# Optimization experiments

Hardware: AMD Instinct MI355X
Metric: run time of the kernel (lower is better)

Reference implementation:

```python
import jax, jax.numpy as jnp
import numpy as np

B, N, DIM, H, DH, K = 4, 2048, 512, 6, 64, 16
KEEP_PROB = 0.9  # 1 - dropout_rate
LOG2PI = float(np.log(2.0 * np.pi))
LOG_PRIOR = float(np.log(1.0 / K))


def setup_inputs() -> dict:
    key = jax.random.key(0)
    ks = jax.random.split(key, 7)
    inputs_q = jax.random.normal(ks[0], (B, N, DIM), dtype=jnp.float32)
    # decoder-style causal mask, shape [B, 1, q_len, kv_len]
    causal = jnp.tril(jnp.ones((N, N), dtype=jnp.float32))
    mask = jnp.broadcast_to(causal[None, None], (B, 1, N, N))
    # dropout keep mask broadcast across the query dim: [B, H, 1, kv_len]
    keep = jax.random.bernoulli(ks[1], KEEP_PROB, (B, H, 1, N)).astype(jnp.float32)
    w_qkv = jax.random.normal(ks[2], (DIM, 3 * H * DH), dtype=jnp.float32) * 0.02
    w_out = jax.random.normal(ks[3], (H * DH, DIM), dtype=jnp.float32) * 0.02
    mu_lookup = jax.random.normal(ks[4], (K, DIM), dtype=jnp.float32)
    logvar_lookup = jax.random.normal(ks[5], (K, DIM), dtype=jnp.float32) * 0.1
    return {
        "inputs_q": inputs_q,
        "mask": mask,
        "keep": keep,
        "w_qkv": w_qkv,
        "w_out": w_out,
        "mu_lookup": mu_lookup,
        "logvar_lookup": logvar_lookup,
    }


def reference(inputs_q, mask, keep, w_qkv, w_out, mu_lookup, logvar_lookup):
    # --- MultiHeadDotProductAttention (self-attn path) ---
    qkv = (inputs_q @ w_qkv).reshape(B, N, 3, H, DH)  # [B,N,3,H,DH]
    q, k, v = qkv[:, :, 0], qkv[:, :, 1], qkv[:, :, 2]
    # bias: 0 where mask > 0, -1e10 elsewhere (note: no 1/sqrt(d) scaling, as in source)
    bias = jnp.where(mask > 0, 0.0, -1e10)
    attn_weights = jnp.einsum('bqhd,bkhd->bhqk', q, k) + bias  # [B,H,N,N]
    attn_weights = jax.nn.softmax(attn_weights, axis=-1)
    # broadcast dropout: mask shared across the query dim
    attn_weights = attn_weights * keep / KEEP_PROB
    attn_out = jnp.einsum('bhqk,bkhd->bqhd', attn_weights, v)
    attn_out = attn_out.reshape(B, N, H * DH) @ w_out  # [B,N,DIM]

    # --- GMM posterior approx q(y|x) ~= p(y|z) (approx_qy_x, vectorized over k) ---
    z = attn_out.mean(axis=1)  # pooled latent, [B,DIM]
    diff = z[:, None, :] - mu_lookup[None]  # [B,K,DIM]
    llh = -0.5 * jnp.sum(
        diff * diff / jnp.exp(logvar_lookup)[None] + logvar_lookup[None] + LOG2PI,
        axis=-1,
    )  # [B,K]
    logLogit_qy_x = llh + LOG_PRIOR
    qy_x = jax.nn.softmax(logLogit_qy_x, axis=1)  # [B,K]

    # combine mixture mean back in so both branches are live in one output
    return attn_out + (qy_x @ mu_lookup)[:, None, :]
```

## Files before the change

kernel.cpp:

```cpp
#include <hip/hip_runtime.h>
#include <cstdint>
#include <cstddef>

#define NH 6
#define NSEQ 2048
#define DIMD 512
#define BATCH 4
#define HD 384
#define LOG2PI_F 1.8378770664093453f
#define LOG2E_F 1.44269504f

typedef __attribute__((ext_vector_type(8))) short short8;
typedef __attribute__((ext_vector_type(8))) unsigned short ushort8;
typedef __attribute__((ext_vector_type(4))) unsigned short ushort4v;
typedef __attribute__((ext_vector_type(4))) float floatx4;
typedef __attribute__((ext_vector_type(2))) unsigned int uint2v;

__device__ inline unsigned short f2bf(float f){
  unsigned int u = __float_as_uint(f);
  u += 0x7FFFu + ((u>>16)&1u);
  return (unsigned short)(u>>16);
}

#define GLD16(gp, lp) __builtin_amdgcn_global_load_lds( \
  (const __attribute__((address_space(1))) void*)(gp), \
  (__attribute__((address_space(3))) void*)(lp), 16, 0, 0)

__global__ __launch_bounds__(256) void prep_kernel(
    const float* __restrict__ xq, const float* __restrict__ wq, const float* __restrict__ wo,
    unsigned short* __restrict__ xbf, unsigned short* __restrict__ wqT,
    unsigned short* __restrict__ woT, float* __restrict__ zA)
{
  __shared__ __attribute__((aligned(16))) unsigned short Ls[64*72];
  const int bid = blockIdx.x, t = threadIdx.x;
  if (bid < 4096){
    int i = bid*256 + t;
    floatx4 v = *(const floatx4*)(xq + (size_t)i*4);
    ushort4v r;
    #pragma unroll
    for(int j=0;j<4;j++) r[j] = f2bf(v[j]);
    *(ushort4v*)(xbf + (size_t)i*4) = r;
  } else if (bid < 4096+144+48){
    const bool isq = bid < 4096+144;
    const int j  = isq ? bid-4096 : bid-(4096+144);
    const int nx = isq ? 18 : 8;
    const int R  = isq ? 512 : 384, C = isq ? 1152 : 512;
    const float* src = isq ? wq : wo;
    unsigned short* dst = isq ? wqT : woT;
    const int x = j % nx, y = j / nx;
    const int n0 = x*64, d0 = y*64;
    const float scale = (isq && n0 < 384) ? LOG2E_F : 1.0f;
    const int r = t>>2, c0 = (t&3)*16;
    #pragma unroll
    for (int jj=0;jj<16;jj+=4){
      floatx4 v = *(const floatx4*)(src + (size_t)(d0+r)*C + n0 + c0 + jj);
      #pragma unroll
      for(int q=0;q<4;q++) Ls[r*72 + c0+jj+q] = f2bf(v[q]*scale);
    }
    __syncthreads();
    #pragma unroll
    for (int jj=0;jj<16;jj+=8){
      ushort8 o;
      #pragma unroll
      for(int q=0;q<8;q++) o[q] = Ls[(c0+jj+q)*72 + r];
      *(ushort8*)(dst + (size_t)(n0+r)*R + d0 + c0 + jj) = o;
    }
  } else {
    for (int i=t; i<BATCH*HD; i+=256) zA[i] = 0.f;
  }
}

__global__ __launch_bounds__(256) void gemm_qkv(
    const unsigned short* __restrict__ A,
    const unsigned short* __restrict__ Bt,
    const float* __restrict__ keep,
    unsigned short* __restrict__ Qo, unsigned short* __restrict__ Ko, unsigned short* __restrict__ Vt)
{
  __shared__ __attribute__((aligned(16))) unsigned short Cs[128*136];
  unsigned short* As = Cs;
  unsigned short* Bs = Cs + 128*64;
  const int tid = threadIdx.x;
  const int w = tid>>6, lane = tid&63;
  const int wr = w>>1, wc = w&1;
  const int quad = lane>>4, l16 = lane&15;
  const int by = blockIdx.y;
  const int tM = blockIdx.x*128, tN = by*128;
  const int r8 = lane>>3, c8 = (lane&7)*8;
  floatx4 acc[4][4];
  floatx4 zed = {0.f,0.f,0.f,0.f};
  #pragma unroll
  for (int i=0;i<4;i++)
    #pragma unroll
    for(int j=0;j<4;j++) acc[i][j] = zed;

  for (int k0=0; k0<512; k0+=64){
    #pragma unroll
    for (int i=0;i<4;i++){
      int row = w*32 + i*8;
      GLD16(A  + (size_t)(tM+row+r8)*512 + k0 + c8, As + row*64);
      GLD16(Bt + (size_t)(tN+row+r8)*512 + k0 + c8, Bs + row*64);
    }
    __syncthreads();
    #pragma unroll
    for (int kk=0; kk<64; kk+=32){
      short8 af[4], bf[4];
      #pragma unroll
      for(int mt=0;mt<4;mt++)
        af[mt] = *(const short8*)(As + (wr*64+mt*16+l16)*64 + kk + quad*8);
      #pragma unroll
      for(int nt=0;nt<4;nt++)
        bf[nt] = *(const short8*)(Bs + (wc*64+nt*16+l16)*64 + kk + quad*8);
      #pragma unroll
      for(int mt=0;mt<4;mt++)
        #pragma unroll
        for(int nt=0;nt<4;nt++)
          acc[mt][nt] = __builtin_amdgcn_mfma_f32_16x16x32_bf16(af[mt], bf[nt], acc[mt][nt], 0,0,0);
    }
    __syncthreads();
  }
  const int b = tM>>11;
  if (by < 6){
    #pragma unroll
    for(int mt=0;mt<4;mt++)
      #pragma unroll
      for(int nt=0;nt<4;nt++)
        #pragma unroll
        for(int r=0;r<4;r++)
          Cs[(wr*64+mt*16+quad*4+r)*132 + wc*64+nt*16+l16] = f2bf(acc[mt][nt][r]);
    __syncthreads();
    const int row = tid>>1, colh = (tid&1)*64;
    const int gcol0 = tN + colh;
    const int tq = gcol0/384, rem = gcol0 - tq*384, h = rem>>6;
    const int grow = tM + row, n = grow & 2047;
    unsigned short* dst = (tq==0 ? Qo : Ko) + ((size_t)((b*NH+h)*NSEQ+n))*64;
    #pragma unroll
    for(int j=0;j<8;j++)
      *(ushort8*)(dst + j*8) = *(const ushort8*)(Cs + row*132 + colh + j*8);
  } else {
    const int hbase = (by-6)*2;
    const float* kp = keep + (size_t)(b*NH + hbase + wc)*NSEQ + (tM & 2047);
    #pragma unroll
    for(int mt=0;mt<4;mt++){
      float kv[4];
      #pragma unroll
      for(int r=0;r<4;r++) kv[r] = kp[wr*64+mt*16+quad*4+r];
      #pragma unroll
      for(int nt=0;nt<4;nt++){
        int col = wc*64+nt*16+l16;
        int row = wr*64+mt*16+quad*4;
        unsigned int lo = (unsigned int)f2bf(acc[mt][nt][0]*kv[0]) | ((unsigned int)f2bf(acc[mt][nt][1]*kv[1])<<16);
        unsigned int hi = (unsigned int)f2bf(acc[mt][nt][2]*kv[2]) | ((unsigned int)f2bf(acc[mt][nt][3]*kv[3])<<16);
        uint2v v2 = {lo, hi};
        *(uint2v*)(Cs + (size_t)col*136 + row) = v2;
      }
    }
    __syncthreads();
    const int nu = tid & 15;
    #pragma unroll
    for(int vc0=0; vc0<128; vc0+=16){
      int vtcol = vc0 + (tid>>4);
      int h2 = hbase + (vtcol>>6), dh = vtcol & 63;
      unsigned short* dstv = Vt + ((size_t)((b*NH+h2)*64 + dh))*NSEQ + (tM & 2047) + nu*8;
      *(ushort8*)dstv = *(const ushort8*)(Cs + (size_t)vtcol*136 + nu*8);
    }
  }
}

__global__ __launch_bounds__(64,2) void attn_kernel(
    const unsigned short* __restrict__ Qg, const unsigned short* __restrict__ Kg,
    const unsigned short* __restrict__ VtG,
    unsigned short* __restrict__ atp,
    float* __restrict__ zA)
{
  __shared__ __attribute__((aligned(16))) unsigned short Ps[64*76];
  const int lane = threadIdx.x;
  const int quad = lane>>4, l16 = lane&15;
  const int bid = blockIdx.x;
  const int idx = bid>>3;
  const int bh  = (bid&7) + 8*(idx % 3);
  const int c   = 31 - idx/3;
  const int b = bh/NH, h = bh - b*NH;
  const unsigned short* Qb = Qg  + (size_t)bh*NSEQ*64;
  const unsigned short* Kb = Kg  + (size_t)bh*NSEQ*64;
  const unsigned short* Vb = VtG + (size_t)bh*64*NSEQ;
  const int q0 = c*64;
  const int nkt = c + 1;

  short8 qf[4][2];
  #pragma unroll
  for(int mt=0;mt<4;mt++)
    #pragma unroll
    for(int kc=0;kc<2;kc++)
      qf[mt][kc] = *(const short8*)(Qb + (size_t)(q0+mt*16+l16)*64 + kc*32 + quad*8);

  short8 onesf;
  #pragma unroll
  for(int j=0;j<8;j++) onesf[j] = (short)0x3F80;

  floatx4 O[4][4];
  floatx4 accl[4];
  floatx4 zed = {0.f,0.f,0.f,0.f};
  #pragma unroll
  for(int mt=0;mt<4;mt++){
    #pragma unroll
    for(int dt=0;dt<4;dt++) O[mt][dt] = zed;
    accl[mt] = zed;
  }

  short8 kf[4][2];
  #pragma unroll
  for(int nt=0;nt<4;nt++)
    #pragma unroll
    for(int kc=0;kc<2;kc++)
      kf[nt][kc] = *(const short8*)(Kb + (size_t)(nt*16+l16)*64 + kc*32 + quad*8);

  for (int kt=0; kt<nkt; kt++){
    const int kB = kt*64;
    short8 vf[2][4];
    const unsigned short* vp0 = Vb + kB;
    #pragma unroll
    for(int kh=0;kh<2;kh++)
      #pragma unroll
      for(int dt=0;dt<4;dt++)
        vf[kh][dt] = *(const short8*)(vp0 + (size_t)(dt*16+l16)*NSEQ + kh*32 + quad*8);

    const bool dia = (kt == nkt-1);
    floatx4 m12 = {-17.3123404907f,-17.3123404907f,-17.3123404907f,-17.3123404907f};
    floatx4 sacc[4];
    #pragma unroll
    for(int mt=0;mt<4;mt++){
      #pragma unroll
      for(int nt=0;nt<4;nt++) sacc[nt] = m12;
      #pragma unroll
      for(int nt=0;nt<4;nt++)
        #pragma unroll
        for(int kc=0;kc<2;kc++)
          sacc[nt] = __builtin_amdgcn_mfma_f32_16x16x32_bf16(qf[mt][kc], kf[nt][kc], sacc[nt], 0,0,0);
      #pragma unroll
      for(int nt=0;nt<4;nt++){
        int key = kB + nt*16 + l16;
        #pragma unroll
        for(int r=0;r<4;r++){
          float p = exp2f(sacc[nt][r]);
          if (dia) p = (key <= q0 + mt*16 + quad*4 + r) ? p : 0.f;
          Ps[(mt*16+quad*4+r)*76 + nt*16 + l16] = (unsigned short)(__float_as_uint(p)>>16);
        }
      }
    }
    if (kt+1 < nkt){
      const unsigned short* kp0 = Kb + (size_t)(kt+1)*64*64;
      #pragma unroll
      for(int nt=0;nt<4;nt++)
        #pragma unroll
        for(int kc=0;kc<2;kc++)
          kf[nt][kc] = *(const short8*)(kp0 + (size_t)(nt*16+l16)*64 + kc*32 + quad*8);
    }
    #pragma unroll
    for(int kh=0;kh<2;kh++){
      #pragma unroll
      for(int mt=0;mt<4;mt++){
        short8 pf = *(const short8*)(Ps + (mt*16+l16)*76 + kh*32 + quad*8);
        accl[mt] = __builtin_amdgcn_mfma_f32_16x16x32_bf16(pf, onesf, accl[mt], 0,0,0);
        #pragma unroll
        for(int dt=0;dt<4;dt++)
          O[mt][dt] = __builtin_amdgcn_mfma_f32_16x16x32_bf16(pf, vf[kh][dt], O[mt][dt], 0,0,0);
      }
    }
  }

  #pragma unroll
  for(int mt=0;mt<4;mt++){
    float sc2[4];
    #pragma unroll
    for(int r=0;r<4;r++) sc2[r] = (1.0f/0.9f) / accl[mt][r];
    #pragma unroll
    for(int dt=0;dt<4;dt++){
      float s = 0.f;
      #pragma unroll
      for(int r=0;r<4;r++){
        float v = O[mt][dt][r]*sc2[r];
        s += v;
        Ps[(mt*16+quad*4+r)*76 + dt*16 + l16] = f2bf(v);
      }
      atomicAdd(&zA[b*HD + h*64 + dt*16 + l16], s);
    }
  }
  unsigned short* dstp = atp + ((size_t)(b*NSEQ + q0 + lane))*HD + h*64;
  #pragma unroll
  for(int j=0;j<4;j++)
    *(ushort8*)(dstp + j*8) = *(const ushort8*)(Ps + lane*76 + j*8);
  #pragma unroll
  for(int j=4;j<8;j++)
    *(ushort8*)(dstp + j*8) = *(const ushort8*)(Ps + lane*76 + j*8);
}

__global__ __launch_bounds__(256) void gmm_kernel(
    const float* __restrict__ zA, const float* __restrict__ wo,
    const float* __restrict__ mu, const float* __restrict__ lv, float* __restrict__ c)
{
  __shared__ float zAs[HD];
  __shared__ float zs[DIMD];
  __shared__ float sh[16];
  __shared__ float qy[16];
  const int tid = threadIdx.x;
  const int b = blockIdx.x;
  for (int i=tid; i<HD; i+=256) zAs[i] = zA[b*HD + i];
  __syncthreads();
  for (int d=tid; d<DIMD; d+=256){
    float s = 0.f;
    for (int k=0; k<HD; k++) s += zAs[k]*wo[(size_t)k*DIMD + d];
    zs[d] = s * (1.0f/2048.0f);
  }
  __syncthreads();
  const int k = tid>>4, li = tid&15;
  float part = 0.f;
  for(int d=li; d<DIMD; d+=16){
    float m = mu[k*DIMD+d], l = lv[k*DIMD+d];
    float diff = zs[d] - m;
    part += diff*diff*__expf(-l) + l + LOG2PI_F;
  }
  #pragma unroll
  for(int off=8;off>=1;off>>=1) part += __shfl_xor(part, off, 64);
  if (li==0) sh[k] = part;
  __syncthreads();
  if (tid<16){
    float logit = -0.5f*sh[tid];
    float mx = logit;
    #pragma unroll
    for(int off=8;off>=1;off>>=1) mx = fmaxf(mx, __shfl_xor(mx, off, 64));
    float e = __expf(logit-mx);
    float se = e;
    #pragma unroll
    for(int off=8;off>=1;off>>=1) se += __shfl_xor(se, off, 64);
    qy[tid] = e/se;
  }
  __syncthreads();
  for(int d=tid; d<DIMD; d+=256){
    float accv = 0.f;
    #pragma unroll
    for(int kk=0;kk<16;kk++) accv += qy[kk]*mu[kk*DIMD+d];
    c[b*DIMD+d] = accv;
  }
}

__global__ __launch_bounds__(256) void gemm_proj(
    const unsigned short* __restrict__ A,
    const unsigned short* __restrict__ Bt,
    const float* __restrict__ c,
    float* __restrict__ out)
{
  __shared__ __attribute__((aligned(16))) unsigned short As[128*64];
  __shared__ __attribute__((aligned(16))) unsigned short Bs[128*64];
  const int tid = threadIdx.x;
  const int w = tid>>6, lane = tid&63;
  const int wr = w>>1, wc = w&1;
  const int quad = lane>>4, l16 = lane&15;
  const int tM = blockIdx.x*128, tN = blockIdx.y*128;
  const int r8 = lane>>3, c8 = (lane&7)*8;
  floatx4 acc[4][4];
  floatx4 zed = {0.f,0.f,0.f,0.f};
  #pragma unroll
  for (int i=0;i<4;i++)
    #pragma unroll
    for(int j=0;j<4;j++) acc[i][j] = zed;

  for (int k0=0; k0<384; k0+=64){
    #pragma unroll
    for (int i=0;i<4;i++){
      int row = w*32 + i*8;
      GLD16(A  + (size_t)(tM+row+r8)*384 + k0 + c8, As + row*64);
      GLD16(Bt + (size_t)(tN+row+r8)*384 + k0 + c8, Bs + row*64);
    }
    __syncthreads();
    #pragma unroll
    for (int kk=0; kk<64; kk+=32){
      short8 af[4], bf[4];
      #pragma unroll
      for(int mt=0;mt<4;mt++)
        af[mt] = *(const short8*)(As + (wr*64+mt*16+l16)*64 + kk + quad*8);
      #pragma unroll
      for(int nt=0;nt<4;nt++)
        bf[nt] = *(const short8*)(Bs + (wc*64+nt*16+l16)*64 + kk + quad*8);
      #pragma unroll
      for(int mt=0;mt<4;mt++)
        #pragma unroll
        for(int nt=0;nt<4;nt++)
          acc[mt][nt] = __builtin_amdgcn_mfma_f32_16x16x32_bf16(af[mt], bf[nt], acc[mt][nt], 0,0,0);
    }
    __syncthreads();
  }
  const int b = tM>>11;
  float cb[4];
  #pragma unroll
  for(int nt=0;nt<4;nt++) cb[nt] = c[b*DIMD + tN + wc*64 + nt*16 + l16];
  #pragma unroll
  for(int mt=0;mt<4;mt++){
    int grow = tM + wr*64 + mt*16 + quad*4;
    #pragma unroll
    for(int nt=0;nt<4;nt++){
      int gcol = tN + wc*64 + nt*16 + l16;
      #pragma unroll
      for(int r=0;r<4;r++)
        out[(size_t)(grow+r)*512 + gcol] = acc[mt][nt][r] + cb[nt];
    }
  }
}

extern "C" void kernel_launch(void* const* d_in, const int* in_sizes, int n_in,
                              void* d_out, int out_size, void* d_ws, size_t ws_size,
                              hipStream_t stream) {
  const float* inputs_q = (const float*)d_in[0];
  const float* keep  = (const float*)d_in[2];
  const float* w_qkv = (const float*)d_in[3];
  const float* w_out = (const float*)d_in[4];
  const float* mu    = (const float*)d_in[5];
  const float* lv    = (const float*)d_in[6];
  float* out = (float*)d_out;
  char* ws = (char*)d_ws;
  size_t off = 0;
  auto alloc = [&](size_t bytes){ void* p = ws + off; off += (bytes + 255) & ~(size_t)255; return p; };
  unsigned short* Qb  = (unsigned short*)alloc((size_t)24*2048*64*2);
  unsigned short* Kb  = (unsigned short*)alloc((size_t)24*2048*64*2);
  unsigned short* Vt  = (unsigned short*)alloc((size_t)24*64*2048*2);
  unsigned short* xbf = (unsigned short*)alloc((size_t)8192*512*2);
  unsigned short* wqT = (unsigned short*)alloc((size_t)1152*512*2);
  unsigned short* woT = (unsigned short*)alloc((size_t)512*384*2);
  unsigned short* atp = (unsigned short*)alloc((size_t)8192*384*2);
  float* zA = (float*)alloc((size_t)4*384*4);
  float* c  = (float*)alloc((size_t)4*512*4);

  prep_kernel<<<4289, 256, 0, stream>>>(inputs_q, w_qkv, w_out, xbf, wqT, woT, zA);
  gemm_qkv<<<dim3(64,9), 256, 0, stream>>>(xbf, wqT, keep, Qb, Kb, Vt);
  attn_kernel<<<768, 64, 0, stream>>>(Qb, Kb, Vt, atp, zA);
  gmm_kernel<<<4, 256, 0, stream>>>(zA, w_out, mu, lv, c);
  gemm_proj<<<dim3(64,4), 256, 0, stream>>>(atp, woT, c, out);
}
```

Baseline: 274.6 us.

## Split attention key range across four waves per block with LDS reduction

Each attention block now uses four wavefronts that each handle a contiguous quarter of the causal key tiles, instead of one wavefront walking all of them. Partial outputs and row sums go to shared memory and are reduced across waves before normalisation, bf16 store, and pooled-sum atomics. This aims to shorten the long serial loop for late query tiles and raise occupancy. The cost is extra LDS traffic, a block barrier, and a possible loss of waves per SIMD from the larger shared footprint.

```diff
diff --git a/kernel.cpp b/kernel.cpp
--- a/kernel.cpp
+++ b/kernel.cpp
@@ -166,14 +166,16 @@
   }
 }
 
-__global__ __launch_bounds__(64,2) void attn_kernel(
+__global__ __launch_bounds__(256,2) void attn_kernel(
     const unsigned short* __restrict__ Qg, const unsigned short* __restrict__ Kg,
     const unsigned short* __restrict__ VtG,
     unsigned short* __restrict__ atp,
     float* __restrict__ zA)
 {
-  __shared__ __attribute__((aligned(16))) unsigned short Ps[64*76];
-  const int lane = threadIdx.x;
+  __shared__ float OpL[4*64*68 + 4*64];
+  float* lP = OpL + 4*64*68;
+  const int tid = threadIdx.x;
+  const int w = tid>>6, lane = tid&63;
   const int quad = lane>>4, l16 = lane&15;
   const int bid = blockIdx.x;
   const int idx = bid>>3;
@@ -185,6 +187,10 @@
   const unsigned short* Vb = VtG + (size_t)bh*64*NSEQ;
   const int q0 = c*64;
   const int nkt = c + 1;
+  const int qch = (nkt+3)>>2;
+  const int t0 = w*qch;
+  const int t1 = min(nkt, t0+qch);
+  unsigned short* Ps = (unsigned short*)(OpL + w*64*68);
 
   short8 qf[4][2];
   #pragma unroll
@@ -207,91 +213,114 @@
     accl[mt] = zed;
   }
 
-  short8 kf[4][2];
-  #pragma unroll
-  for(int nt=0;nt<4;nt++)
-    #pragma unroll
-    for(int kc=0;kc<2;kc++)
-      kf[nt][kc] = *(const short8*)(Kb + (size_t)(nt*16+l16)*64 + kc*32 + quad*8);
-
-  for (int kt=0; kt<nkt; kt++){
-    const int kB = kt*64;
-    short8 vf[2][4];
-    const unsigned short* vp0 = Vb + kB;
-    #pragma unroll
-    for(int kh=0;kh<2;kh++)
-      #pragma unroll
-      for(int dt=0;dt<4;dt++)
-        vf[kh][dt] = *(const short8*)(vp0 + (size_t)(dt*16+l16)*NSEQ + kh*32 + quad*8);
-
-    const bool dia = (kt == nkt-1);
-    floatx4 m12 = {-17.3123404907f,-17.3123404907f,-17.3123404907f,-17.3123404907f};
-    floatx4 sacc[4];
-    #pragma unroll
-    for(int mt=0;mt<4;mt++){
-      #pragma unroll
-      for(int nt=0;nt<4;nt++) sacc[nt] = m12;
-      #pragma unroll
-      for(int nt=0;nt<4;nt++)
-        #pragma unroll
-        for(int kc=0;kc<2;kc++)
-          sacc[nt] = __builtin_amdgcn_mfma_f32_16x16x32_bf16(qf[mt][kc], kf[nt][kc], sacc[nt], 0,0,0);
-      #pragma unroll
-      for(int nt=0;nt<4;nt++){
-        int key = kB + nt*16 + l16;
-        #pragma unroll
-        for(int r=0;r<4;r++){
-          float p = exp2f(sacc[nt][r]);
-          if (dia) p = (key <= q0 + mt*16 + quad*4 + r) ? p : 0.f;
-          Ps[(mt*16+quad*4+r)*76 + nt*16 + l16] = (unsigned short)(__float_as_uint(p)>>16);
+  if (t0 < t1){
+    short8 kf[4][2];
+    #pragma unroll
+    for(int nt=0;nt<4;nt++)
+      #pragma unroll
+      for(int kc=0;kc<2;kc++)
+        kf[nt][kc] = *(const short8*)(Kb + (size_t)(t0*64 + nt*16+l16)*64 + kc*32 + quad*8);
+
+    for (int kt=t0; kt<t1; kt++){
+      const int kB = kt*64;
+      short8 vf[2][4];
+      const unsigned short* vp0 = Vb + kB;
+      #pragma unroll
+      for(int kh=0;kh<2;kh++)
+        #pragma unroll
+        for(int dt=0;dt<4;dt++)
+          vf[kh][dt] = *(const short8*)(vp0 + (size_t)(dt*16+l16)*NSEQ + kh*32 + quad*8);
+
+      const bool dia = (kt == nkt-1);
+      floatx4 m12 = {-17.3123404907f,-17.3123404907f,-17.3123404907f,-17.3123404907f};
+      floatx4 sacc[4];
+      #pragma unroll
+      for(int mt=0;mt<4;mt++){
+        #pragma unroll
+        for(int nt=0;nt<4;nt++) sacc[nt] = m12;
+        #pragma unroll
+        for(int nt=0;nt<4;nt++)
+          #pragma unroll
+          for(int kc=0;kc<2;kc++)
+            sacc[nt] = __builtin_amdgcn_mfma_f32_16x16x32_bf16(qf[mt][kc], kf[nt][kc], sacc[nt], 0,0,0);
+        #pragma unroll
+        for(int nt=0;nt<4;nt++){
+          int key = kB + nt*16 + l16;
+          #pragma unroll
+          for(int r=0;r<4;r++){
+            float p = exp2f(sacc[nt][r]);
+            if (dia) p = (key <= q0 + mt*16 + quad*4 + r) ? p : 0.f;
+            Ps[(mt*16+quad*4+r)*76 + nt*16 + l16] = (unsigned short)(__float_as_uint(p)>>16);
+          }
         }
       }
-    }
-    if (kt+1 < nkt){
-      const unsigned short* kp0 = Kb + (size_t)(kt+1)*64*64;
-      #pragma unroll
-      for(int nt=0;nt<4;nt++)
-        #pragma unroll
-        for(int kc=0;kc<2;kc++)
-          kf[nt][kc] = *(const short8*)(kp0 + (size_t)(nt*16+l16)*64 + kc*32 + quad*8);
-    }
-    #pragma unroll
-    for(int kh=0;kh<2;kh++){
-      #pragma unroll
-      for(int mt=0;mt<4;mt++){
-        short8 pf = *(const short8*)(Ps + (mt*16+l16)*76 + kh*32 + quad*8);
-        accl[mt] = __builtin_amdgcn_mfma_f32_16x16x32_bf16(pf, onesf, accl[mt], 0,0,0);
-        #pragma unroll
-        for(int dt=0;dt<4;dt++)
-          O[mt][dt] = __builtin_amdgcn_mfma_f32_16x16x32_bf16(pf, vf[kh][dt], O[mt][dt], 0,0,0);
+      if (kt+1 < t1){
+        const unsigned short* kp0 = Kb + (size_t)(kt+1)*64*64;
+        #pragma unroll
+        for(int nt=0;nt<4;nt++)
+          #pragma unroll
+          for(int kc=0;kc<2;kc++)
+            kf[nt][kc] = *(const short8*)(kp0 + (size_t)(nt*16+l16)*64 + kc*32 + quad*8);
       }
-    }
-  }
-
+      #pragma unroll
+      for(int kh=0;kh<2;kh++){
+        #pragma unroll
+        for(int mt=0;mt<4;mt++){
+          short8 pf = *(const short8*)(Ps + (mt*16+l16)*76 + kh*32 + quad*8);
+          accl[mt] = __builtin_amdgcn_mfma_f32_16x16x32_bf16(pf, onesf, accl[mt], 0,0,0);
+          #pragma unroll
+          for(int dt=0;dt<4;dt++)
+            O[mt][dt] = __builtin_amdgcn_mfma_f32_16x16x32_bf16(pf, vf[kh][dt], O[mt][dt], 0,0,0);
+        }
+      }
+    }
+  }
+
+  float* OpW = OpL + w*64*68;
   #pragma unroll
   for(int mt=0;mt<4;mt++){
-    float sc2[4];
-    #pragma unroll
-    for(int r=0;r<4;r++) sc2[r] = (1.0f/0.9f) / accl[mt][r];
-    #pragma unroll
-    for(int dt=0;dt<4;dt++){
-      float s = 0.f;
-      #pragma unroll
-      for(int r=0;r<4;r++){
-        float v = O[mt][dt][r]*sc2[r];
-        s += v;
-        Ps[(mt*16+quad*4+r)*76 + dt*16 + l16] = f2bf(v);
-      }
-      atomicAdd(&zA[b*HD + h*64 + dt*16 + l16], s);
-    }
-  }
-  unsigned short* dstp = atp + ((size_t)(b*NSEQ + q0 + lane))*HD + h*64;
-  #pragma unroll
-  for(int j=0;j<4;j++)
-    *(ushort8*)(dstp + j*8) = *(const ushort8*)(Ps + lane*76 + j*8);
-  #pragma unroll
-  for(int j=4;j<8;j++)
-    *(ushort8*)(dstp + j*8) = *(const ushort8*)(Ps + lane*76 + j*8);
+    #pragma unroll
+    for(int r=0;r<4;r++){
+      if (l16 == 0) lP[w*64 + mt*16+quad*4+r] = accl[mt][r];
+      #pragma unroll
+      for(int dt=0;dt<4;dt++)
+        OpW[(mt*16+quad*4+r)*68 + dt*16+l16] = O[mt][dt][r];
+    }
+  }
+  __syncthreads();
+
+  const int r2 = w*16 + (lane>>2);
+  const int s  = (lane&3)*16;
+  float lt = lP[r2] + lP[64+r2] + lP[128+r2] + lP[192+r2];
+  float sc2 = (1.0f/0.9f)/lt;
+  float v[16];
+  #pragma unroll
+  for(int p=0;p<4;p++){
+    const float* Pp = OpL + p*64*68 + r2*68 + s;
+    #pragma unroll
+    for(int j=0;j<4;j++){
+      floatx4 t4 = *(const floatx4*)(Pp + j*4);
+      if (p==0){ v[j*4]=t4[0]; v[j*4+1]=t4[1]; v[j*4+2]=t4[2]; v[j*4+3]=t4[3]; }
+      else     { v[j*4]+=t4[0]; v[j*4+1]+=t4[1]; v[j*4+2]+=t4[2]; v[j*4+3]+=t4[3]; }
+    }
+  }
+  #pragma unroll
+  for(int j=0;j<16;j++) v[j] *= sc2;
+  ushort8 o0, o1;
+  #pragma unroll
+  for(int j=0;j<8;j++){ o0[j] = f2bf(v[j]); o1[j] = f2bf(v[8+j]); }
+  unsigned short* dp = atp + ((size_t)(b*NSEQ + q0 + r2))*HD + h*64 + s;
+  *(ushort8*)dp = o0;
+  *(ushort8*)(dp+8) = o1;
+  #pragma unroll
+  for(int j=0;j<16;j++){
+    float zv = v[j];
+    zv += __shfl_xor(zv, 4, 64);
+    zv += __shfl_xor(zv, 8, 64);
+    zv += __shfl_xor(zv, 16, 64);
+    zv += __shfl_xor(zv, 32, 64);
+    if ((lane>>2)==0) atomicAdd(&zA[b*HD + h*64 + s + j], zv);
+  }
 }
 
 __global__ __launch_bounds__(256) void gmm_kernel(
@@ -431,7 +460,7 @@
 
   prep_kernel<<<4289, 256, 0, stream>>>(inputs_q, w_qkv, w_out, xbf, wqT, woT, zA);
   gemm_qkv<<<dim3(64,9), 256, 0, stream>>>(xbf, wqT, keep, Qb, Kb, Vt);
-  attn_kernel<<<768, 64, 0, stream>>>(Qb, Kb, Vt, atp, zA);
+  attn_kernel<<<768, 256, 0, stream>>>(Qb, Kb, Vt, atp, zA);
   gmm_kernel<<<4, 256, 0, stream>>>(zA, w_out, mu, lv, c);
   gemm_proj<<<dim3(64,4), 256, 0, stream>>>(atp, woT, c, out);
 }
```

Measured after the change: 284.1 us. 3.4% more time.

## Stage K/V tiles in double-buffered LDS shared by two waves per block

Applied to the files above, without the earlier changes.

The attention kernel now runs two wavefronts per block, each handling 32 query rows of the 64-row tile. K and V tiles are loaded into double-buffered shared memory with direct global-to-LDS loads and an XOR swizzle, so the next tile's fetch overlaps the current tile's compute. The two waves share each K/V tile, which halves global K/V traffic per query. V's row stride is padded to 2176 to spread accesses across channels. The cost is a block barrier per tile and more LDS per block, which may lower occupancy.

```diff
diff --git a/kernel.cpp b/kernel.cpp
--- a/kernel.cpp
+++ b/kernel.cpp
@@ -4,6 +4,7 @@
 
 #define NH 6
 #define NSEQ 2048
+#define NS2 2176
 #define DIMD 512
 #define BATCH 4
 #define HD 384
@@ -160,20 +161,23 @@
     for(int vc0=0; vc0<128; vc0+=16){
       int vtcol = vc0 + (tid>>4);
       int h2 = hbase + (vtcol>>6), dh = vtcol & 63;
-      unsigned short* dstv = Vt + ((size_t)((b*NH+h2)*64 + dh))*NSEQ + (tM & 2047) + nu*8;
+      unsigned short* dstv = Vt + ((size_t)((b*NH+h2)*64 + dh))*NS2 + (tM & 2047) + nu*8;
       *(ushort8*)dstv = *(const ushort8*)(Cs + (size_t)vtcol*136 + nu*8);
     }
   }
 }
 
-__global__ __launch_bounds__(64,2) void attn_kernel(
+__global__ __launch_bounds__(128) void attn_kernel(
     const unsigned short* __restrict__ Qg, const unsigned short* __restrict__ Kg,
     const unsigned short* __restrict__ VtG,
     unsigned short* __restrict__ atp,
     float* __restrict__ zA)
 {
-  __shared__ __attribute__((aligned(16))) unsigned short Ps[64*76];
-  const int lane = threadIdx.x;
+  __shared__ __attribute__((aligned(16))) unsigned short Ks[2][64*64];
+  __shared__ __attribute__((aligned(16))) unsigned short Vs[2][64*64];
+  __shared__ __attribute__((aligned(16))) unsigned short Ps[2*32*76];
+  const int tid = threadIdx.x;
+  const int w = tid>>6, lane = tid&63;
   const int quad = lane>>4, l16 = lane&15;
   const int bid = blockIdx.x;
   const int idx = bid>>3;
@@ -182,13 +186,16 @@
   const int b = bh/NH, h = bh - b*NH;
   const unsigned short* Qb = Qg  + (size_t)bh*NSEQ*64;
   const unsigned short* Kb = Kg  + (size_t)bh*NSEQ*64;
-  const unsigned short* Vb = VtG + (size_t)bh*64*NSEQ;
-  const int q0 = c*64;
+  const unsigned short* Vb = VtG + (size_t)bh*64*NS2;
+  const int q0 = c*64 + w*32;
   const int nkt = c + 1;
-
-  short8 qf[4][2];
-  #pragma unroll
-  for(int mt=0;mt<4;mt++)
+  const int gr = lane>>3;
+  const int sc = ((lane&7) ^ gr)*8;
+  const int sw = l16&7;
+
+  short8 qf[2][2];
+  #pragma unroll
+  for(int mt=0;mt<2;mt++)
     #pragma unroll
     for(int kc=0;kc<2;kc++)
       qf[mt][kc] = *(const short8*)(Qb + (size_t)(q0+mt*16+l16)*64 + kc*32 + quad*8);
@@ -197,69 +204,84 @@
   #pragma unroll
   for(int j=0;j<8;j++) onesf[j] = (short)0x3F80;
 
-  floatx4 O[4][4];
-  floatx4 accl[4];
+  floatx4 O[2][4];
+  floatx4 accl[2];
   floatx4 zed = {0.f,0.f,0.f,0.f};
   #pragma unroll
-  for(int mt=0;mt<4;mt++){
+  for(int mt=0;mt<2;mt++){
     #pragma unroll
     for(int dt=0;dt<4;dt++) O[mt][dt] = zed;
     accl[mt] = zed;
   }
-
-  short8 kf[4][2];
-  #pragma unroll
-  for(int nt=0;nt<4;nt++)
-    #pragma unroll
-    for(int kc=0;kc<2;kc++)
-      kf[nt][kc] = *(const short8*)(Kb + (size_t)(nt*16+l16)*64 + kc*32 + quad*8);
-
+  unsigned short* Pw = Ps + w*32*76;
+
+  auto stage = [&](int kt, int bb){
+    const int kB = kt*64;
+    unsigned short* Kd = Ks[bb];
+    unsigned short* Vd = Vs[bb];
+    #pragma unroll
+    for(int i=0;i<4;i++){
+      int r0 = i*16 + w*8;
+      GLD16(Kb + (size_t)(kB + r0 + gr)*64 + sc, Kd + r0*64);
+      GLD16(Vb + (size_t)(r0 + gr)*NS2 + kB + sc, Vd + r0*64);
+    }
+  };
+
+  stage(0, 0);
   for (int kt=0; kt<nkt; kt++){
+    const int cur = kt&1;
+    __syncthreads();
+    if (kt+1 < nkt) stage(kt+1, cur^1);
+    const unsigned short* Kd = Ks[cur];
+    const unsigned short* Vd = Vs[cur];
     const int kB = kt*64;
-    short8 vf[2][4];
-    const unsigned short* vp0 = Vb + kB;
-    #pragma unroll
-    for(int kh=0;kh<2;kh++)
-      #pragma unroll
-      for(int dt=0;dt<4;dt++)
-        vf[kh][dt] = *(const short8*)(vp0 + (size_t)(dt*16+l16)*NSEQ + kh*32 + quad*8);
+
+    short8 kf[4][2];
+    #pragma unroll
+    for(int nt=0;nt<4;nt++)
+      #pragma unroll
+      for(int kc=0;kc<2;kc++)
+        kf[nt][kc] = *(const short8*)(Kd + (nt*16+l16)*64 + (((kc*4+quad) ^ sw)<<3));
+
+    floatx4 m12 = {-17.3123404907f,-17.3123404907f,-17.3123404907f,-17.3123404907f};
+    floatx4 sacc[2][4];
+    #pragma unroll
+    for(int mt=0;mt<2;mt++)
+      #pragma unroll
+      for(int nt=0;nt<4;nt++) sacc[mt][nt] = m12;
+    #pragma unroll
+    for(int mt=0;mt<2;mt++)
+      #pragma unroll
+      for(int nt=0;nt<4;nt++)
+        #pragma unroll
+        for(int kc=0;kc<2;kc++)
+          sacc[mt][nt] = __builtin_amdgcn_mfma_f32_16x16x32_bf16(qf[mt][kc], kf[nt][kc], sacc[mt][nt], 0,0,0);
 
     const bool dia = (kt == nkt-1);
-    floatx4 m12 = {-17.3123404907f,-17.3123404907f,-17.3123404907f,-17.3123404907f};
-    floatx4 sacc[4];
-    #pragma unroll
-    for(int mt=0;mt<4;mt++){
-      #pragma unroll
-      for(int nt=0;nt<4;nt++) sacc[nt] = m12;
-      #pragma unroll
-      for(int nt=0;nt<4;nt++)
-        #pragma unroll
-        for(int kc=0;kc<2;kc++)
-          sacc[nt] = __builtin_amdgcn_mfma_f32_16x16x32_bf16(qf[mt][kc], kf[nt][kc], sacc[nt], 0,0,0);
+    #pragma unroll
+    for(int mt=0;mt<2;mt++){
       #pragma unroll
       for(int nt=0;nt<4;nt++){
         int key = kB + nt*16 + l16;
         #pragma unroll
         for(int r=0;r<4;r++){
-          float p = exp2f(sacc[nt][r]);
+          float p = exp2f(sacc[mt][nt][r]);
           if (dia) p = (key <= q0 + mt*16 + quad*4 + r) ? p : 0.f;
-          Ps[(mt*16+quad*4+r)*76 + nt*16 + l16] = (unsigned short)(__float_as_uint(p)>>16);
+          Pw[(mt*16+quad*4+r)*76 + nt*16 + l16] = (unsigned short)(__float_as_uint(p)>>16);
         }
       }
     }
-    if (kt+1 < nkt){
-      const unsigned short* kp0 = Kb + (size_t)(kt+1)*64*64;
-      #pragma unroll
-      for(int nt=0;nt<4;nt++)
-        #pragma unroll
-        for(int kc=0;kc<2;kc++)
-          kf[nt][kc] = *(const short8*)(kp0 + (size_t)(nt*16+l16)*64 + kc*32 + quad*8);
-    }
+    short8 vf[2][4];
+    #pragma unroll
+    for(int kh=0;kh<2;kh++)
+      #pragma unroll
+      for(int dt=0;dt<4;dt++)
+        vf[kh][dt] = *(const short8*)(Vd + (dt*16+l16)*64 + (((kh*4+quad) ^ sw)<<3));
     #pragma unroll
     for(int kh=0;kh<2;kh++){
       #pragma unroll
-      for(int mt=0;mt<4;mt++){
-        short8 pf = *(const short8*)(Ps + (mt*16+l16)*76 + kh*32 + quad*8);
+      for(int mt=0;mt<2;mt++){
+        short8 pf = *(const short8*)(Pw + (mt*16+l16)*76 + kh*32 + quad*8);
         accl[mt] = __builtin_amdgcn_mfma_f32_16x16x32_bf16(pf, onesf, accl[mt], 0,0,0);
         #pragma unroll
         for(int dt=0;dt<4;dt++)
@@ -269,7 +291,7 @@
   }
 
   #pragma unroll
-  for(int mt=0;mt<4;mt++){
+  for(int mt=0;mt<2;mt++){
     float sc2[4];
     #pragma unroll
     for(int r=0;r<4;r++) sc2[r] = (1.0f/0.9f) / accl[mt][r];
@@ -280,18 +302,16 @@
       for(int r=0;r<4;r++){
         float v = O[mt][dt][r]*sc2[r];
         s += v;
-        Ps[(mt*16+quad*4+r)*76 + dt*16 + l16] = f2bf(v);
+        Pw[(mt*16+quad*4+r)*76 + dt*16 + l16] = f2bf(v);
       }
       atomicAdd(&zA[b*HD + h*64 + dt*16 + l16], s);
     }
   }
-  unsigned short* dstp = atp + ((size_t)(b*NSEQ + q0 + lane))*HD + h*64;
+  const int rr = lane>>1, half = (lane&1)*32;
+  unsigned short* dp = atp + ((size_t)(b*NSEQ + q0 + rr))*HD + h*64 + half;
   #pragma unroll
   for(int j=0;j<4;j++)
-    *(ushort8*)(dstp + j*8) = *(const ushort8*)(Ps + lane*76 + j*8);
-  #pragma unroll
-  for(int j=4;j<8;j++)
-    *(ushort8*)(dstp + j*8) = *(const ushort8*)(Ps + lane*76 + j*8);
+    *(ushort8*)(dp + j*8) = *(const ushort8*)(Pw + rr*76 + half + j*8);
 }
 
 __global__ __launch_bounds__(256) void gmm_kernel(
@@ -421,7 +441,7 @@
   auto alloc = [&](size_t bytes){ void* p = ws + off; off += (bytes + 255) & ~(size_t)255; return p; };
   unsigned short* Qb  = (unsigned short*)alloc((size_t)24*2048*64*2);
   unsigned short* Kb  = (unsigned short*)alloc((size_t)24*2048*64*2);
-  unsigned short* Vt  = (unsigned short*)alloc((size_t)24*64*2048*2);
+  unsigned short* Vt  = (unsigned short*)alloc((size_t)24*64*NS2*2);
   unsigned short* xbf = (unsigned short*)alloc((size_t)8192*512*2);
   unsigned short* wqT = (unsigned short*)alloc((size_t)1152*512*2);
   unsigned short* woT = (unsigned short*)alloc((size_t)512*384*2);
@@ -431,7 +451,7 @@
 
   prep_kernel<<<4289, 256, 0, stream>>>(inputs_q, w_qkv, w_out, xbf, wqT, woT, zA);
   gemm_qkv<<<dim3(64,9), 256, 0, stream>>>(xbf, wqT, keep, Qb, Kb, Vt);
-  attn_kernel<<<768, 64, 0, stream>>>(Qb, Kb, Vt, atp, zA);
+  attn_kernel<<<768, 128, 0, stream>>>(Qb, Kb, Vt, atp, zA);
   gmm_kernel<<<4, 256, 0, stream>>>(zA, w_out, mu, lv, c);
   gemm_proj<<<dim3(64,4), 256, 0, stream>>>(atp, woT, c, out);
 }
```

New measurement: 259.6 us. 1.06x faster.
